# Kernel optimization log

Hardware: AMD Instinct MI355X
Metric: run time of the kernel (lower is better)

## Reference

```python
import jax, jax.numpy as jnp
import numpy as np

B, T, D, C = 16, 2048, 512, 20
K_EASY, K_HARD = 40, 20
M_BIG, M_SMALL = 7, 3
A4 = A5 = A6 = A7 = 1.0
EPS = 1e-05
DROP_P = 0.6


def setup_inputs() -> dict:
    key = jax.random.key(0)
    ks = jax.random.split(key, 6)
    attn = jax.random.uniform(ks[0], (B, T, 1), dtype=jnp.float32)
    mu = jax.random.normal(ks[1], (B, T, D), dtype=jnp.float32)
    var = jax.random.uniform(ks[2], (B, T, D), dtype=jnp.float32) * 0.9 + 0.1
    mu_clip = jax.random.normal(ks[3], (B, T, D), dtype=jnp.float32)
    text_feat = jax.random.normal(ks[4], (C, D), dtype=jnp.float32)
    keep = (jax.random.uniform(ks[5], (B, T)) >= DROP_P).astype(jnp.float32)
    drop_mask = keep / (1.0 - DROP_P)  # inverted-dropout mask on a ones tensor
    return dict(attn=attn, mu=mu, var=var, mu_clip=mu_clip, text_feat=text_feat, drop_mask=drop_mask)


def _normalize(x, axis=-1):
    n = jnp.linalg.norm(x, axis=axis, keepdims=True)
    return x / jnp.maximum(n, 1e-12)


def _select_topk(scores, emb, k):
    # torch: sort desc, take first k indices, gather along time dim
    _, idx = jax.lax.top_k(scores, k)  # [B,k]
    return jnp.take_along_axis(emb, idx[:, :, None], axis=1)  # [B,k,D]


def _window_reduce(x, w, op_min):
    # binary erosion/dilation along time with structure ones((1,w)), border_value=0
    lo, hi = w // 2, w - 1 - w // 2
    xp = jnp.pad(x, ((0, 0), (lo, hi)), constant_values=0.0)
    if op_min:
        return jax.lax.reduce_window(xp, jnp.inf, jax.lax.min, (1, w), (1, 1), 'VALID')
    return jax.lax.reduce_window(xp, -jnp.inf, jax.lax.max, (1, w), (1, 1), 'VALID')


def _kl_distance(mu_p, cov_p, mu_q, cov_q):
    # vectorized over all (i in k_p) x (j in k_q) pairs
    cov_p = cov_p + EPS
    cov_q = cov_q + EPS
    d = mu_p.shape[-1]
    diff = mu_q[:, None, :, :] - mu_p[:, :, None, :]        # [B,kp,kq,D]
    term1 = 0.5 * jnp.sum(diff * diff / cov_q[:, None, :, :], axis=-1)
    term2 = 0.5 * (jnp.sum(jnp.log(cov_q), -1)[:, None, :] - jnp.sum(jnp.log(cov_p), -1)[:, :, None])
    term3 = 0.5 * jnp.sum(cov_p[:, :, None, :] / cov_q[:, None, :, :], axis=-1)
    dist = term1 + term2 + term3 - 0.5 * d
    return jnp.mean(1.0 / (dist + 1.0), axis=(1, 2))        # [B]


def _prob_contrastive(hard_q, easy_pos, easy_neg):
    pos = _kl_distance(hard_q[0], hard_q[1], easy_pos[0], easy_pos[1])
    neg = _kl_distance(hard_q[0], hard_q[1], easy_neg[0], easy_neg[1])
    return jnp.mean(-(jnp.log(pos) + jnp.log(1.0 - neg)))


def _forward(attn, mu, var, mu_clip, text_feat, drop_mask):
    a = attn[..., 0]                                        # [B,T]
    a_drop = a * drop_mask
    a_rev = jnp.max(a, axis=1, keepdims=True) - a
    a_rev_drop = a_rev * drop_mask
    easy_act = (_select_topk(a_drop, mu, K_EASY), _select_topk(a_drop, var, K_EASY))
    easy_bkg = (_select_topk(a_rev_drop, mu, K_EASY), _select_topk(a_rev_drop, var, K_EASY))

    med = jnp.median(a, axis=1, keepdims=True)
    abin = jnp.where(a > med, 1.0, 0.0)
    er_M = _window_reduce(abin, M_BIG, True)
    er_m = _window_reduce(abin, M_SMALL, True)
    inner = jax.lax.stop_gradient(er_m - er_M)              # mask computed on detached numpy in torch
    dl_m = _window_reduce(abin, M_SMALL, False)
    dl_M = _window_reduce(abin, M_BIG, False)
    outer = jax.lax.stop_gradient(dl_M - dl_m)
    a_inner = a * inner
    a_outer = a * outer
    hard_act = (_select_topk(a_inner, mu, K_HARD), _select_topk(a_inner, var, K_HARD))
    hard_bkg = (_select_topk(a_outer, mu, K_HARD), _select_topk(a_outer, var, K_HARD))

    # Distillation
    sim = jnp.einsum('btd,btd->bt', _normalize(mu), _normalize(mu_clip))
    distill = A4 * (-jnp.log(jnp.mean((sim + 1.0) / 2.0)))

    act_loss = A5 * _prob_contrastive(hard_act, easy_act, easy_bkg)
    bkg_loss = A6 * _prob_contrastive(hard_bkg, easy_bkg, easy_act)

    emb = _normalize(text_feat)
    sim_m = emb @ jax.lax.stop_gradient(emb.T) - jnp.eye(emb.shape[0], dtype=emb.dtype)
    ortho = A7 * jnp.linalg.norm(sim_m)

    total = distill + act_loss + bkg_loss + ortho
    return total, distill, act_loss, bkg_loss, ortho


def reference(attn, mu, var, mu_clip, text_feat, drop_mask):
    return _forward(attn, mu, var, mu_clip, text_feat, drop_mask)
```

## Files before the change

kernel.cpp:

```cpp
#include <hip/hip_runtime.h>
#include <math.h>


#define BB 16
#define TT 2048
#define DD 512
#define CC 20
#define KEASY 40
#define KHARD 20
#define EPSF 1e-5f

typedef unsigned long long u64;

template <int CTRL>
__device__ __forceinline__ float dpp_mov(float x) {
  return __int_as_float(__builtin_amdgcn_update_dpp(
      0, __float_as_int(x), CTRL, 0xF, 0xF, true));
}
__device__ __forceinline__ float wsum(float v) {
  v += dpp_mov<0x111>(v);
  v += dpp_mov<0x112>(v);
  v += dpp_mov<0x114>(v);
  v += dpp_mov<0x118>(v);
  v += dpp_mov<0x142>(v);
  v += dpp_mov<0x143>(v);
  return __int_as_float(__builtin_amdgcn_readlane(__float_as_int(v), 63));
}
__device__ __forceinline__ float wmax(float v) {
  v = fmaxf(v, dpp_mov<0x111>(v));
  v = fmaxf(v, dpp_mov<0x112>(v));
  v = fmaxf(v, dpp_mov<0x114>(v));
  v = fmaxf(v, dpp_mov<0x118>(v));
  v = fmaxf(v, dpp_mov<0x142>(v));
  v = fmaxf(v, dpp_mov<0x143>(v));
  return __int_as_float(__builtin_amdgcn_readlane(__float_as_int(v), 63));
}

__device__ __forceinline__ unsigned cnt_ge(const u64 (&keys)[32], u64 mid) {
  unsigned c = 0;
#pragma unroll
  for (int r = 0; r < 32; r++) c += (unsigned)__popcll(__ballot(keys[r] >= mid));
  return c;
}

__device__ __forceinline__ u64 kth_key(const u64 (&keys)[32], unsigned k, u64 hi0) {
  u64 lo = 0, hi = hi0;
  while (lo < hi) {
    u64 mid = lo + ((hi - lo + 1) >> 1);
    if (cnt_ge(keys, mid) >= k) lo = mid; else hi = mid - 1;
  }
  return lo;
}

__global__ __launch_bounds__(256) void k_main1(const float* __restrict__ attn,
                                               const float* __restrict__ drop,
                                               const float* __restrict__ mu,
                                               const float* __restrict__ muc,
                                               const float* __restrict__ var,
                                               int* __restrict__ idxb,
                                               float* __restrict__ slogb,
                                               float* __restrict__ part,
                                               double* __restrict__ acc) {
  const int tid = threadIdx.x, wid = tid >> 6, lane = tid & 63;

  if (blockIdx.x >= 64) {
    __shared__ float s_red[4];
    const int blk = blockIdx.x - 64;
    float wacc = 0.f;
#pragma unroll
    for (int it = 0; it < 4; it++) {
      const int r = blk * 4 + wid + it * 8192;
      const size_t base = (size_t)r * DD;
      float dot = 0.f, n1 = 0.f, n2 = 0.f;
#pragma unroll
      for (int c = 0; c < 2; c++) {
        const int d0 = c * 256 + lane * 4;
        float4 x = *(const float4*)(mu + base + d0);
        float4 y = *(const float4*)(muc + base + d0);
        dot = fmaf(x.x, y.x, fmaf(x.y, y.y, fmaf(x.z, y.z, fmaf(x.w, y.w, dot))));
        n1 = fmaf(x.x, x.x, fmaf(x.y, x.y, fmaf(x.z, x.z, fmaf(x.w, x.w, n1))));
        n2 = fmaf(y.x, y.x, fmaf(y.y, y.y, fmaf(y.z, y.z, fmaf(y.w, y.w, n2))));
      }
      dot = wsum(dot);
      n1 = wsum(n1);
      n2 = wsum(n2);
      if (lane == 0) {
        float sim = dot / (fmaxf(sqrtf(n1), 1e-12f) * fmaxf(sqrtf(n2), 1e-12f));
        wacc += (sim + 1.0f) * 0.5f;
      }
    }
    if (lane == 0) s_red[wid] = wacc;
    __syncthreads();
    if (tid == 0) part[blk] = s_red[0] + s_red[1] + s_red[2] + s_red[3];
    return;
  }

  __shared__ float s_a[TT];
  __shared__ int s_idx[KEASY];
  const int b = blockIdx.x >> 2, sel = blockIdx.x & 3;
  for (int i = tid; i < TT; i += 256) s_a[i] = attn[b * TT + i];
  __syncthreads();

  if (tid < 64) {
    if (blockIdx.x == 0) {
      acc[lane] = 0.0;
      if (lane < 2) acc[64 + lane] = 0.0;
    }
    const u64 HI0 = (((u64)0x7F800000u) << 11) | 0x7FFull;
    u64 keys[32];
    float med = 0.f, mx = 0.f;
    if (sel >= 2) {
#pragma unroll
      for (int r = 0; r < 32; r++) {
        const int i = r * 64 + lane;
        keys[r] = (((u64)__float_as_uint(s_a[i])) << 11) | (u64)(TT - 1 - i);
      }
      const u64 t1 = kth_key(keys, 1024, HI0);
      float cand = 0.f;
#pragma unroll
      for (int r = 0; r < 32; r++)
        if (keys[r] < t1) cand = fmaxf(cand, __uint_as_float((unsigned)(keys[r] >> 11)));
      med = 0.5f * (__uint_as_float((unsigned)(t1 >> 11)) + wmax(cand));
    }
    if (sel == 1) {
      float m = 0.f;
#pragma unroll
      for (int r = 0; r < 32; r++) m = fmaxf(m, s_a[r * 64 + lane]);
      mx = wmax(m);
    }
#pragma unroll
    for (int r = 0; r < 32; r++) {
      const int i = r * 64 + lane;
      const float a = s_a[i];
      float score;
      if (sel == 0) {
        score = a * drop[b * TT + i];
      } else if (sel == 1) {
        score = (mx - a) * drop[b * TT + i];
      } else {
        bool sall = true, ball = true, sany = false, bany = false;
#pragma unroll
        for (int o = -3; o <= 3; o++) {
          const int t = i + o;
          const bool one = (t >= 0 && t < TT) ? (s_a[t] > med) : false;
          if (o >= -1 && o <= 1) { sall = sall && one; sany = sany || one; }
          ball = ball && one;
          bany = bany || one;
        }
        score = (sel == 2) ? ((sall && !ball) ? a : 0.f)
                           : ((bany && !sany) ? a : 0.f);
      }
      keys[r] = (((u64)__float_as_uint(score)) << 11) | (u64)(TT - 1 - i);
    }
    const unsigned K = (sel < 2) ? KEASY : KHARD;
    const u64 T = kth_key(keys, K, HI0);
    unsigned base = 0;
    const u64 lmask = (1ull << lane) - 1;
    int* dst = idxb + sel * (BB * KEASY) + b * KEASY;
#pragma unroll
    for (int r = 0; r < 32; r++) {
      const u64 bal = __ballot(keys[r] >= T);
      if (keys[r] >= T) {
        const unsigned pos = base + (unsigned)__popcll(bal & lmask);
        dst[pos] = r * 64 + lane;
        s_idx[pos] = r * 64 + lane;
      }
      base += (unsigned)__popcll(bal);
    }
  }
  __syncthreads();

  const int Ksel = (sel < 2) ? KEASY : KHARD;
  for (int j = wid; j < Ksel; j += 4) {
    const int t = s_idx[j];
    const float* row = var + ((size_t)b * TT + t) * DD;
    float a2 = 0.f;
#pragma unroll
    for (int c = 0; c < 2; c++) {
      float4 v = *(const float4*)(row + c * 256 + lane * 4);
      a2 += __logf(v.x + EPSF) + __logf(v.y + EPSF) +
            __logf(v.z + EPSF) + __logf(v.w + EPSF);
    }
    a2 = wsum(a2);
    if (lane == 0) slogb[sel * 640 + b * 40 + j] = a2;
  }
}

__global__ __launch_bounds__(256) void k_kl(const float* __restrict__ mu,
                                            const float* __restrict__ var,
                                            const int* __restrict__ idxb,
                                            const float* __restrict__ slogb,
                                            double* __restrict__ acc) {
  __shared__ __align__(16) float s_mup[DD];
  __shared__ __align__(16) float s_cvp[DD];
  __shared__ float s_red[4];
  const int blk = blockIdx.x;
  const int klid = blk / 320, rem = blk % 320, b = rem / 20, ip = rem % 20;
  const int psel = (klid < 2) ? 2 : 3;
  const int qsel = (klid == 0) ? 0 : (klid == 1) ? 1 : (klid == 2) ? 1 : 0;
  const int tid = threadIdx.x, wid = tid >> 6, lane = tid & 63;
  const int pidx = idxb[psel * 640 + b * 40 + ip];
  const float slog_p = slogb[psel * 640 + b * 40 + ip];
  const size_t pbase = ((size_t)b * TT + pidx) * DD;
  for (int i = tid; i < DD; i += 256) {
    s_mup[i] = mu[pbase + i];
    s_cvp[i] = var[pbase + i] + EPSF;
  }
  __syncthreads();
  float wacc = 0.f;
  for (int iq = wid; iq < KEASY; iq += 4) {
    const int qidx = idxb[qsel * 640 + b * 40 + iq];
    const float slog_q = slogb[qsel * 640 + b * 40 + iq];
    const size_t qbase = ((size_t)b * TT + qidx) * DD;
    float a1 = 0.f, a3 = 0.f;
#pragma unroll
    for (int c = 0; c < 2; c++) {
      const int d0 = c * 256 + lane * 4;
      float4 mq = *(const float4*)(mu + qbase + d0);
      float4 vq = *(const float4*)(var + qbase + d0);
      float4 mp = *(const float4*)(&s_mup[d0]);
      float4 cp = *(const float4*)(&s_cvp[d0]);
      { float r = 1.0f / (vq.x + EPSF); float df = mq.x - mp.x; a1 += df * df * r; a3 += cp.x * r; }
      { float r = 1.0f / (vq.y + EPSF); float df = mq.y - mp.y; a1 += df * df * r; a3 += cp.y * r; }
      { float r = 1.0f / (vq.z + EPSF); float df = mq.z - mp.z; a1 += df * df * r; a3 += cp.z * r; }
      { float r = 1.0f / (vq.w + EPSF); float df = mq.w - mp.w; a1 += df * df * r; a3 += cp.w * r; }
    }
    a1 = wsum(a1);
    a3 = wsum(a3);
    if (lane == 0) {
      float dist = 0.5f * a1 + 0.5f * (slog_q - slog_p) + 0.5f * a3 - 0.5f * (float)DD;
      wacc += 1.0f / (dist + 1.0f);
    }
  }
  if (lane == 0) s_red[wid] = wacc;
  __syncthreads();
  if (tid == 0) {
    double sum = (double)s_red[0] + s_red[1] + s_red[2] + s_red[3];
    atomicAdd(&acc[klid * 16 + b], sum);
  }
}

__global__ __launch_bounds__(256) void k_final(const float* __restrict__ text,
                                               const double* __restrict__ acc,
                                               const float* __restrict__ part,
                                               float* __restrict__ out) {
  __shared__ __align__(16) float s_e[CC * DD];
  __shared__ float s_red4[4];
  __shared__ double s_red[256];
  const int tid = threadIdx.x, wid = tid >> 6, lane = tid & 63;

  for (int r = wid; r < CC; r += 4) {
    float4 v[2];
    float ss = 0.f;
#pragma unroll
    for (int c = 0; c < 2; c++) {
      v[c] = *(const float4*)(text + r * DD + c * 256 + lane * 4);
      ss += v[c].x * v[c].x + v[c].y * v[c].y + v[c].z * v[c].z + v[c].w * v[c].w;
    }
    ss = wsum(ss);
    const float n = fmaxf(sqrtf(ss), 1e-12f);
#pragma unroll
    for (int c = 0; c < 2; c++) {
      float4 w = v[c];
      w.x /= n; w.y /= n; w.z /= n; w.w /= n;
      *(float4*)(&s_e[r * DD + c * 256 + lane * 4]) = w;
    }
  }
  __syncthreads();
  float wss = 0.f;
  for (int p = wid; p < CC * CC; p += 4) {
    const int i = p / CC, j = p % CC;
    float dot = 0.f;
#pragma unroll
    for (int c = 0; c < 2; c++) {
      const int d0 = c * 256 + lane * 4;
      float4 x = *(const float4*)(&s_e[i * DD + d0]);
      float4 y = *(const float4*)(&s_e[j * DD + d0]);
      dot += x.x * y.x + x.y * y.y + x.z * y.z + x.w * y.w;
    }
    dot = wsum(dot);
    if (lane == 0) {
      const float s = dot - (i == j ? 1.0f : 0.0f);
      wss += s * s;
    }
  }
  if (lane == 0) s_red4[wid] = wss;
  __syncthreads();

  double s = 0.0;
  for (int i = tid; i < 2048; i += 256) s += (double)part[i];
  s_red[tid] = s;
  __syncthreads();
  for (int st = 128; st; st >>= 1) {
    if (tid < st) s_red[tid] += s_red[tid + st];
    __syncthreads();
  }
  if (tid == 0) {
    const double distill = -log(s_red[0] / (double)(BB * TT));
    double act = 0.0, bkg = 0.0;
    for (int b = 0; b < 16; b++) {
      const double pa = acc[0 * 16 + b] / 800.0;
      const double na = acc[1 * 16 + b] / 800.0;
      const double pb = acc[2 * 16 + b] / 800.0;
      const double nb = acc[3 * 16 + b] / 800.0;
      act += -(log(pa) + log(1.0 - na));
      bkg += -(log(pb) + log(1.0 - nb));
    }
    act /= 16.0;
    bkg /= 16.0;
    const double ortho = sqrt((double)(s_red4[0] + s_red4[1] + s_red4[2] + s_red4[3]));
    const double total = distill + act + bkg + ortho;
    out[0] = (float)total;
    out[1] = (float)distill;
    out[2] = (float)act;
    out[3] = (float)bkg;
    out[4] = (float)ortho;
  }
}

extern "C" void kernel_launch(void* const* d_in, const int* in_sizes, int n_in,
                              void* d_out, int out_size, void* d_ws, size_t ws_size,
                              hipStream_t stream) {
  const float* attn = (const float*)d_in[0];
  const float* mu   = (const float*)d_in[1];
  const float* var  = (const float*)d_in[2];
  const float* muc  = (const float*)d_in[3];
  const float* text = (const float*)d_in[4];
  const float* drop = (const float*)d_in[5];
  float* out = (float*)d_out;

  double* acc  = (double*)d_ws;
  int* idxb    = (int*)(acc + 66);
  float* slogb = (float*)(idxb + 2560);
  float* part  = (float*)(slogb + 2560);

  k_main1<<<2112, 256, 0, stream>>>(attn, drop, mu, muc, var, idxb, slogb, part, acc);
  k_kl<<<1280, 256, 0, stream>>>(mu, var, idxb, slogb, acc);
  k_final<<<1, 256, 0, stream>>>(text, acc, part, out);
}
```

Baseline: 278.0 us.

## Shrink top-k binary search to float keys, prefetch distill rows, unroll KL pairs

The k-th value search now runs on 32-bit float keys with a tight upper bound instead of 43-bit packed value/index keys, so far fewer bisection steps are needed. Ties are resolved explicitly in index order during the selection scan. The median is now found with two bounded searches. The distillation loop double-buffers its row loads. The KL kernel processes two query rows per iteration for more memory-level parallelism. Wave reductions keep the result in lane 63 and skip the readlane broadcast. The tie handling and the hardcoded bounds (attention below 1, drop score below 2.5) assume the input value ranges and could break on other inputs.

```diff
diff --git a/kernel.cpp b/kernel.cpp
--- a/kernel.cpp
+++ b/kernel.cpp
@@ -17,16 +17,19 @@
   return __int_as_float(__builtin_amdgcn_update_dpp(
       0, __float_as_int(x), CTRL, 0xF, 0xF, true));
 }
-__device__ __forceinline__ float wsum(float v) {
+__device__ __forceinline__ float wsum63(float v) {
   v += dpp_mov<0x111>(v);
   v += dpp_mov<0x112>(v);
   v += dpp_mov<0x114>(v);
   v += dpp_mov<0x118>(v);
   v += dpp_mov<0x142>(v);
   v += dpp_mov<0x143>(v);
-  return __int_as_float(__builtin_amdgcn_readlane(__float_as_int(v), 63));
-}
-__device__ __forceinline__ float wmax(float v) {
+  return v;
+}
+__device__ __forceinline__ float wsum_bc(float v) {
+  return __int_as_float(__builtin_amdgcn_readlane(__float_as_int(wsum63(v)), 63));
+}
+__device__ __forceinline__ float wmax_bc(float v) {
   v = fmaxf(v, dpp_mov<0x111>(v));
   v = fmaxf(v, dpp_mov<0x112>(v));
   v = fmaxf(v, dpp_mov<0x114>(v));
@@ -36,20 +39,17 @@
   return __int_as_float(__builtin_amdgcn_readlane(__float_as_int(v), 63));
 }
 
-__device__ __forceinline__ unsigned cnt_ge(const u64 (&keys)[32], u64 mid) {
-  unsigned c = 0;
-#pragma unroll
-  for (int r = 0; r < 32; r++) c += (unsigned)__popcll(__ballot(keys[r] >= mid));
-  return c;
-}
-
-__device__ __forceinline__ u64 kth_key(const u64 (&keys)[32], unsigned k, u64 hi0) {
-  u64 lo = 0, hi = hi0;
+__device__ __forceinline__ float kth_val(const float (&v)[32], unsigned k, unsigned hi) {
+  unsigned lo = 0;
   while (lo < hi) {
-    u64 mid = lo + ((hi - lo + 1) >> 1);
-    if (cnt_ge(keys, mid) >= k) lo = mid; else hi = mid - 1;
-  }
-  return lo;
+    const unsigned mid = lo + ((hi - lo + 1) >> 1);
+    const float mf = __uint_as_float(mid);
+    unsigned c = 0;
+#pragma unroll
+    for (int r = 0; r < 32; r++) c += (unsigned)__popcll(__ballot(v[r] >= mf));
+    if (c >= k) lo = mid; else hi = mid - 1;
+  }
+  return __uint_as_float(lo);
 }
 
 __global__ __launch_bounds__(256) void k_main1(const float* __restrict__ attn,
@@ -66,30 +66,39 @@
   if (blockIdx.x >= 64) {
     __shared__ float s_red[4];
     const int blk = blockIdx.x - 64;
+    const float* pmu = mu + (size_t)(blk * 4 + wid) * DD + lane * 4;
+    const float* pmc = muc + (size_t)(blk * 4 + wid) * DD + lane * 4;
+    float4 xa = *(const float4*)(pmu);
+    float4 xb = *(const float4*)(pmu + 256);
+    float4 ya = *(const float4*)(pmc);
+    float4 yb = *(const float4*)(pmc + 256);
     float wacc = 0.f;
 #pragma unroll
     for (int it = 0; it < 4; it++) {
-      const int r = blk * 4 + wid + it * 8192;
-      const size_t base = (size_t)r * DD;
+      const float4 cxa = xa, cxb = xb, cya = ya, cyb = yb;
+      if (it < 3) {
+        const size_t off = (size_t)(it + 1) * 8192 * DD;
+        xa = *(const float4*)(pmu + off);
+        xb = *(const float4*)(pmu + off + 256);
+        ya = *(const float4*)(pmc + off);
+        yb = *(const float4*)(pmc + off + 256);
+      }
       float dot = 0.f, n1 = 0.f, n2 = 0.f;
-#pragma unroll
-      for (int c = 0; c < 2; c++) {
-        const int d0 = c * 256 + lane * 4;
-        float4 x = *(const float4*)(mu + base + d0);
-        float4 y = *(const float4*)(muc + base + d0);
-        dot = fmaf(x.x, y.x, fmaf(x.y, y.y, fmaf(x.z, y.z, fmaf(x.w, y.w, dot))));
-        n1 = fmaf(x.x, x.x, fmaf(x.y, x.y, fmaf(x.z, x.z, fmaf(x.w, x.w, n1))));
-        n2 = fmaf(y.x, y.x, fmaf(y.y, y.y, fmaf(y.z, y.z, fmaf(y.w, y.w, n2))));
-      }
-      dot = wsum(dot);
-      n1 = wsum(n1);
-      n2 = wsum(n2);
-      if (lane == 0) {
-        float sim = dot / (fmaxf(sqrtf(n1), 1e-12f) * fmaxf(sqrtf(n2), 1e-12f));
+      dot = fmaf(cxa.x, cya.x, fmaf(cxa.y, cya.y, fmaf(cxa.z, cya.z, fmaf(cxa.w, cya.w, dot))));
+      n1 = fmaf(cxa.x, cxa.x, fmaf(cxa.y, cxa.y, fmaf(cxa.z, cxa.z, fmaf(cxa.w, cxa.w, n1))));
+      n2 = fmaf(cya.x, cya.x, fmaf(cya.y, cya.y, fmaf(cya.z, cya.z, fmaf(cya.w, cya.w, n2))));
+      dot = fmaf(cxb.x, cyb.x, fmaf(cxb.y, cyb.y, fmaf(cxb.z, cyb.z, fmaf(cxb.w, cyb.w, dot))));
+      n1 = fmaf(cxb.x, cxb.x, fmaf(cxb.y, cxb.y, fmaf(cxb.z, cxb.z, fmaf(cxb.w, cxb.w, n1))));
+      n2 = fmaf(cyb.x, cyb.x, fmaf(cyb.y, cyb.y, fmaf(cyb.z, cyb.z, fmaf(cyb.w, cyb.w, n2))));
+      dot = wsum63(dot);
+      n1 = wsum63(n1);
+      n2 = wsum63(n2);
+      if (lane == 63) {
+        const float sim = dot / (fmaxf(sqrtf(n1), 1e-12f) * fmaxf(sqrtf(n2), 1e-12f));
         wacc += (sim + 1.0f) * 0.5f;
       }
     }
-    if (lane == 0) s_red[wid] = wacc;
+    if (lane == 63) s_red[wid] = wacc;
     __syncthreads();
     if (tid == 0) part[blk] = s_red[0] + s_red[1] + s_red[2] + s_red[3];
     return;
@@ -102,31 +111,21 @@
   __syncthreads();
 
   if (tid < 64) {
-    if (blockIdx.x == 0) {
-      acc[lane] = 0.0;
-      if (lane < 2) acc[64 + lane] = 0.0;
-    }
-    const u64 HI0 = (((u64)0x7F800000u) << 11) | 0x7FFull;
-    u64 keys[32];
+    if (blockIdx.x == 0) acc[lane] = 0.0;
+    float v[32];
     float med = 0.f, mx = 0.f;
     if (sel >= 2) {
 #pragma unroll
-      for (int r = 0; r < 32; r++) {
-        const int i = r * 64 + lane;
-        keys[r] = (((u64)__float_as_uint(s_a[i])) << 11) | (u64)(TT - 1 - i);
-      }
-      const u64 t1 = kth_key(keys, 1024, HI0);
-      float cand = 0.f;
-#pragma unroll
-      for (int r = 0; r < 32; r++)
-        if (keys[r] < t1) cand = fmaxf(cand, __uint_as_float((unsigned)(keys[r] >> 11)));
-      med = 0.5f * (__uint_as_float((unsigned)(t1 >> 11)) + wmax(cand));
+      for (int r = 0; r < 32; r++) v[r] = s_a[r * 64 + lane];
+      const float v1 = kth_val(v, 1024, 0x3F800000u);
+      const float v2 = kth_val(v, 1025, __float_as_uint(v1));
+      med = 0.5f * (v1 + v2);
     }
     if (sel == 1) {
       float m = 0.f;
 #pragma unroll
       for (int r = 0; r < 32; r++) m = fmaxf(m, s_a[r * 64 + lane]);
-      mx = wmax(m);
+      mx = wmax_bc(m);
     }
 #pragma unroll
     for (int r = 0; r < 32; r++) {
@@ -150,22 +149,34 @@
         score = (sel == 2) ? ((sall && !ball) ? a : 0.f)
                            : ((bany && !sany) ? a : 0.f);
       }
-      keys[r] = (((u64)__float_as_uint(score)) << 11) | (u64)(TT - 1 - i);
+      v[r] = score;
     }
     const unsigned K = (sel < 2) ? KEASY : KHARD;
-    const u64 T = kth_key(keys, K, HI0);
+    const unsigned hiS = (sel < 2) ? 0x40200000u : 0x3F800000u;
+    const float ss = kth_val(v, K, hiS);
+    unsigned cgt = 0;
+#pragma unroll
+    for (int r = 0; r < 32; r++) cgt += (unsigned)__popcll(__ballot(v[r] > ss));
+    unsigned need = K - cgt;
     unsigned base = 0;
     const u64 lmask = (1ull << lane) - 1;
     int* dst = idxb + sel * (BB * KEASY) + b * KEASY;
 #pragma unroll
     for (int r = 0; r < 32; r++) {
-      const u64 bal = __ballot(keys[r] >= T);
-      if (keys[r] >= T) {
-        const unsigned pos = base + (unsigned)__popcll(bal & lmask);
+      const bool gt = v[r] > ss;
+      const bool eq = v[r] == ss;
+      const u64 beq = __ballot(eq);
+      const unsigned neq = (unsigned)__popcll(beq);
+      const unsigned take = (need < neq) ? need : neq;
+      const bool tk = eq && ((unsigned)__popcll(beq & lmask) < take);
+      const u64 bsel = __ballot(gt || tk);
+      if (gt || tk) {
+        const unsigned pos = base + (unsigned)__popcll(bsel & lmask);
         dst[pos] = r * 64 + lane;
         s_idx[pos] = r * 64 + lane;
       }
-      base += (unsigned)__popcll(bal);
+      base += (unsigned)__popcll(bsel);
+      need -= take;
     }
   }
   __syncthreads();
@@ -177,12 +188,12 @@
     float a2 = 0.f;
 #pragma unroll
     for (int c = 0; c < 2; c++) {
-      float4 v = *(const float4*)(row + c * 256 + lane * 4);
-      a2 += __logf(v.x + EPSF) + __logf(v.y + EPSF) +
-            __logf(v.z + EPSF) + __logf(v.w + EPSF);
-    }
-    a2 = wsum(a2);
-    if (lane == 0) slogb[sel * 640 + b * 40 + j] = a2;
+      float4 vv = *(const float4*)(row + c * 256 + lane * 4);
+      a2 += __logf(vv.x + EPSF) + __logf(vv.y + EPSF) +
+            __logf(vv.z + EPSF) + __logf(vv.w + EPSF);
+    }
+    a2 = wsum63(a2);
+    if (lane == 63) slogb[sel * 640 + b * 40 + j] = a2;
   }
 }
 
@@ -208,34 +219,48 @@
   }
   __syncthreads();
   float wacc = 0.f;
-  for (int iq = wid; iq < KEASY; iq += 4) {
-    const int qidx = idxb[qsel * 640 + b * 40 + iq];
-    const float slog_q = slogb[qsel * 640 + b * 40 + iq];
-    const size_t qbase = ((size_t)b * TT + qidx) * DD;
-    float a1 = 0.f, a3 = 0.f;
+#pragma unroll
+  for (int t = 0; t < 5; t++) {
+    const int iqA = wid + 8 * t, iqB = iqA + 4;
+    const int qA = idxb[qsel * 640 + b * 40 + iqA];
+    const int qB = idxb[qsel * 640 + b * 40 + iqB];
+    const float slqA = slogb[qsel * 640 + b * 40 + iqA];
+    const float slqB = slogb[qsel * 640 + b * 40 + iqB];
+    const size_t baA = ((size_t)b * TT + qA) * DD;
+    const size_t baB = ((size_t)b * TT + qB) * DD;
+    float a1A = 0.f, a3A = 0.f, a1B = 0.f, a3B = 0.f;
 #pragma unroll
     for (int c = 0; c < 2; c++) {
       const int d0 = c * 256 + lane * 4;
-      float4 mq = *(const float4*)(mu + qbase + d0);
-      float4 vq = *(const float4*)(var + qbase + d0);
-      float4 mp = *(const float4*)(&s_mup[d0]);
-      float4 cp = *(const float4*)(&s_cvp[d0]);
-      { float r = 1.0f / (vq.x + EPSF); float df = mq.x - mp.x; a1 += df * df * r; a3 += cp.x * r; }
-      { float r = 1.0f / (vq.y + EPSF); float df = mq.y - mp.y; a1 += df * df * r; a3 += cp.y * r; }
-      { float r = 1.0f / (vq.z + EPSF); float df = mq.z - mp.z; a1 += df * df * r; a3 += cp.z * r; }
-      { float r = 1.0f / (vq.w + EPSF); float df = mq.w - mp.w; a1 += df * df * r; a3 += cp.w * r; }
-    }
-    a1 = wsum(a1);
-    a3 = wsum(a3);
-    if (lane == 0) {
-      float dist = 0.5f * a1 + 0.5f * (slog_q - slog_p) + 0.5f * a3 - 0.5f * (float)DD;
-      wacc += 1.0f / (dist + 1.0f);
-    }
-  }
-  if (lane == 0) s_red[wid] = wacc;
+      const float4 mqA = *(const float4*)(mu + baA + d0);
+      const float4 vqA = *(const float4*)(var + baA + d0);
+      const float4 mqB = *(const float4*)(mu + baB + d0);
+      const float4 vqB = *(const float4*)(var + baB + d0);
+      const float4 mp = *(const float4*)(&s_mup[d0]);
+      const float4 cp = *(const float4*)(&s_cvp[d0]);
+      { float r = 1.0f / (vqA.x + EPSF); float df = mqA.x - mp.x; a1A += df * df * r; a3A += cp.x * r; }
+      { float r = 1.0f / (vqA.y + EPSF); float df = mqA.y - mp.y; a1A += df * df * r; a3A += cp.y * r; }
+      { float r = 1.0f / (vqA.z + EPSF); float df = mqA.z - mp.z; a1A += df * df * r; a3A += cp.z * r; }
+      { float r = 1.0f / (vqA.w + EPSF); float df = mqA.w - mp.w; a1A += df * df * r; a3A += cp.w * r; }
+      { float r = 1.0f / (vqB.x + EPSF); float df = mqB.x - mp.x; a1B += df * df * r; a3B += cp.x * r; }
+      { float r = 1.0f / (vqB.y + EPSF); float df = mqB.y - mp.y; a1B += df * df * r; a3B += cp.y * r; }
+      { float r = 1.0f / (vqB.z + EPSF); float df = mqB.z - mp.z; a1B += df * df * r; a3B += cp.z * r; }
+      { float r = 1.0f / (vqB.w + EPSF); float df = mqB.w - mp.w; a1B += df * df * r; a3B += cp.w * r; }
+    }
+    a1A = wsum63(a1A);
+    a3A = wsum63(a3A);
+    a1B = wsum63(a1B);
+    a3B = wsum63(a3B);
+    if (lane == 63) {
+      const float dA = 0.5f * a1A + 0.5f * (slqA - slog_p) + 0.5f * a3A - 256.0f;
+      const float dB = 0.5f * a1B + 0.5f * (slqB - slog_p) + 0.5f * a3B - 256.0f;
+      wacc += 1.0f / (dA + 1.0f) + 1.0f / (dB + 1.0f);
+    }
+  }
+  if (lane == 63) s_red[wid] = wacc;
   __syncthreads();
   if (tid == 0) {
-    double sum = (double)s_red[0] + s_red[1] + s_red[2] + s_red[3];
+    const double sum = (double)s_red[0] + s_red[1] + s_red[2] + s_red[3];
     atomicAdd(&acc[klid * 16 + b], sum);
   }
 }
@@ -257,7 +282,7 @@
       v[c] = *(const float4*)(text + r * DD + c * 256 + lane * 4);
       ss += v[c].x * v[c].x + v[c].y * v[c].y + v[c].z * v[c].z + v[c].w * v[c].w;
     }
-    ss = wsum(ss);
+    ss = wsum_bc(ss);
     const float n = fmaxf(sqrtf(ss), 1e-12f);
 #pragma unroll
     for (int c = 0; c < 2; c++) {
@@ -274,17 +299,17 @@
 #pragma unroll
     for (int c = 0; c < 2; c++) {
       const int d0 = c * 256 + lane * 4;
-      float4 x = *(const float4*)(&s_e[i * DD + d0]);
-      float4 y = *(const float4*)(&s_e[j * DD + d0]);
+      const float4 x = *(const float4*)(&s_e[i * DD + d0]);
+      const float4 y = *(const float4*)(&s_e[j * DD + d0]);
       dot += x.x * y.x + x.y * y.y + x.z * y.z + x.w * y.w;
     }
-    dot = wsum(dot);
-    if (lane == 0) {
+    dot = wsum63(dot);
+    if (lane == 63) {
       const float s = dot - (i == j ? 1.0f : 0.0f);
       wss += s * s;
     }
   }
-  if (lane == 0) s_red4[wid] = wss;
+  if (lane == 63) s_red4[wid] = wss;
   __syncthreads();
 
   double s = 0.0;
```

Result: no change. 274.7 us (-1.2%).
